# Kernel tuning notes

Measured on AMD Instinct MI355X. Metric: run time of the kernel, lower is better.

Reference implementation:

```python
import jax, jax.numpy as jnp
import numpy as np

N_NODES = 50000
N_EDGES = 800000
IN_C = 256
HID_C = 256
OUT_C = 128
N_GRAPHS = 256


def setup_inputs() -> dict:
    key = jax.random.key(0)
    ks = jax.random.split(key, 12)
    x = jax.random.normal(ks[0], (N_NODES, IN_C), dtype=jnp.float32)
    src = jax.random.randint(ks[1], (N_EDGES,), 0, N_NODES, dtype=jnp.int32)
    dst = jnp.sort(jax.random.randint(ks[2], (N_EDGES,), 0, N_NODES, dtype=jnp.int32))
    p = jax.random.uniform(ks[3], (N_NODES,), dtype=jnp.float32)
    batch = jnp.sort(jax.random.randint(ks[4], (N_NODES,), 0, N_GRAPHS, dtype=jnp.int32))
    root_ptr = jax.random.randint(ks[5], (N_GRAPHS,), 0, N_NODES, dtype=jnp.int32)
    s1 = 1.0 / np.sqrt(IN_C)
    s2 = 1.0 / np.sqrt(HID_C)
    s3 = 1.0 / np.sqrt(2 * HID_C)
    Wl1 = jax.random.uniform(ks[6], (IN_C, HID_C), jnp.float32, -s1, s1)
    Wr1 = jax.random.uniform(ks[7], (IN_C, HID_C), jnp.float32, -s1, s1)
    b1 = jnp.zeros((HID_C,), jnp.float32)
    Wl2 = jax.random.uniform(ks[8], (HID_C, HID_C), jnp.float32, -s2, s2)
    Wr2 = jax.random.uniform(ks[9], (HID_C, HID_C), jnp.float32, -s2, s2)
    b2 = jnp.zeros((HID_C,), jnp.float32)
    Wlin = jax.random.uniform(ks[10], (2 * HID_C, OUT_C), jnp.float32, -s3, s3)
    blin = jax.random.uniform(ks[11], (OUT_C,), jnp.float32, -s3, s3)
    return {"x": x, "src": src, "dst": dst, "p": p, "batch": batch,
            "root_ptr": root_ptr, "num_graphs": N_GRAPHS,
            "Wl1": Wl1, "Wr1": Wr1, "b1": b1,
            "Wl2": Wl2, "Wr2": Wr2, "b2": b2,
            "Wlin": Wlin, "blin": blin}


def _sage_conv(x, src, dst, inv_deg, Wl, Wr, b):
    # mean aggregation of neighbor features: scatter-add then divide by degree
    agg = jax.ops.segment_sum(x[src], dst, num_segments=N_NODES)  # [N, d]
    agg = agg * inv_deg[:, None]
    return agg @ Wl + x @ Wr + b


def reference(x, src, dst, p, batch, root_ptr, num_graphs,
              Wl1, Wr1, b1, Wl2, Wr2, b2, Wlin, blin):
    # in-degree for mean aggregation (shared by both convs)
    deg = jax.ops.segment_sum(jnp.ones_like(dst, dtype=x.dtype), dst,
                              num_segments=N_NODES)
    inv_deg = jnp.where(deg > 0, 1.0 / jnp.maximum(deg, 1.0), 0.0)

    h = _sage_conv(x, src, dst, inv_deg, Wl1, Wr1, b1)
    h = jax.nn.relu(h)  # dropout is identity in eval mode
    h = _sage_conv(h, src, dst, inv_deg, Wl2, Wr2, b2)

    # masked mean pool of p-weighted features per graph
    pw = h * p[:, None]
    gsum = jax.ops.segment_sum(pw, batch, num_segments=num_graphs)
    gcnt = jax.ops.segment_sum(jnp.ones_like(p), batch, num_segments=num_graphs)
    gmean = gsum / jnp.maximum(gcnt, 1.0)[:, None]

    feat = jnp.concatenate([h[root_ptr], gmean], axis=-1)  # [G, 2*hid]
    return feat @ Wlin + blin
```

## Files before the change

### kernel.cpp

```cpp
#include <hip/hip_runtime.h>
#include <hip/hip_bf16.h>

#define N_NODES 50000
#define N_EDGES 800000
#define C_DIM   256
#define OUT_C   128
#define N_GRAPHS 256

typedef unsigned short ushort8 __attribute__((ext_vector_type(8)));
typedef __bf16         bf16x8  __attribute__((ext_vector_type(8)));
typedef float          f32x4   __attribute__((ext_vector_type(4)));

typedef __attribute__((address_space(1))) const unsigned int gu32;
typedef __attribute__((address_space(3))) unsigned int lu32;

#if __has_builtin(__builtin_amdgcn_sched_barrier)
#define SCHED_FENCE() __builtin_amdgcn_sched_barrier(0)
#else
#define SCHED_FENCE() ((void)0)
#endif

__device__ __forceinline__ float us2f(unsigned short u) {
    unsigned int x = ((unsigned int)u) << 16;
    return __builtin_bit_cast(float, x);
}
__device__ __forceinline__ unsigned short f2bf(float f) {
    unsigned int u = __builtin_bit_cast(unsigned int, f);
    u += 0x7fffu + ((u >> 16) & 1u);
    return (unsigned short)(u >> 16);
}

__device__ __forceinline__ int lower_bound_i(const int* __restrict__ a, int n, int v) {
    int lo = 0, hi = n;
    while (lo < hi) {
        int mid = (lo + hi) >> 1;
        if (a[mid] < v) lo = mid + 1; else hi = mid;
    }
    return lo;
}

__global__ void build_ptrs(const int* __restrict__ dst, const int* __restrict__ batch,
                           int* __restrict__ row_ptr, int* __restrict__ graph_ptr,
                           float* __restrict__ inv_deg) {
    int i = blockIdx.x * blockDim.x + threadIdx.x;
    if (i <= N_NODES) {
        int lb = lower_bound_i(dst, N_EDGES, i);
        row_ptr[i] = lb;
        if (i < N_NODES) {
            int ub = lower_bound_i(dst, N_EDGES, i + 1);
            int cnt = ub - lb;
            inv_deg[i] = (cnt > 0) ? (1.0f / (float)cnt) : 0.0f;
        }
    }
    if (i <= N_GRAPHS) graph_ptr[i] = lower_bound_i(batch, N_NODES, i);
}

__global__ void convert_bf16(const float* __restrict__ S, unsigned short* __restrict__ D) {
    int i = blockIdx.x * blockDim.x + threadIdx.x;
    float4 v = *(const float4*)(S + ((size_t)i << 2));
    ushort4 o;
    o.x = f2bf(v.x); o.y = f2bf(v.y); o.z = f2bf(v.z); o.w = f2bf(v.w);
    *(ushort4*)(D + ((size_t)i << 2)) = o;
}

__global__ void transpose256x4(const float* __restrict__ S0, const float* __restrict__ S1,
                               const float* __restrict__ S2, const float* __restrict__ S3,
                               unsigned short* __restrict__ D0, unsigned short* __restrict__ D1,
                               unsigned short* __restrict__ D2, unsigned short* __restrict__ D3) {
    const float* S; unsigned short* D;
    switch (blockIdx.y) {
        case 0: S = S0; D = D0; break;
        case 1: S = S1; D = D1; break;
        case 2: S = S2; D = D2; break;
        default: S = S3; D = D3; break;
    }
    int i = blockIdx.x * 256 + threadIdx.x;
    int k = i >> 8, n = i & 255;
    D[n * 256 + k] = f2bf(S[i]);
}

__global__ void aggregate(const unsigned short* __restrict__ X,
                          const int* __restrict__ src,
                          const int* __restrict__ row_ptr,
                          const float* __restrict__ inv_deg,
                          unsigned short* __restrict__ out) {
    int gw   = (blockIdx.x * blockDim.x + threadIdx.x) >> 6;
    int lane = threadIdx.x & 63;
    if (gw >= N_NODES) return;
    int e0 = row_ptr[gw], e1 = row_ptr[gw + 1];
    const int lo = lane << 2;
    float a0 = 0.f, a1 = 0.f, a2 = 0.f, a3 = 0.f;
    int e = e0;

    for (; e + 16 <= e1; e += 16) {
        int sidx[16];
#pragma unroll
        for (int j = 0; j < 16; ++j) sidx[j] = src[e + j];
        ushort4 v[16];
#pragma unroll
        for (int j = 0; j < 16; ++j)
            v[j] = *(const ushort4*)(X + ((size_t)sidx[j] << 8) + lo);
        SCHED_FENCE();
#pragma unroll
        for (int j = 0; j < 16; ++j) {
            a0 += us2f(v[j].x); a1 += us2f(v[j].y);
            a2 += us2f(v[j].z); a3 += us2f(v[j].w);
        }
    }
    int rem = e1 - e;
    if (rem > 0) {
        int cl = e1 - 1;
        int sidx[16]; float w[16];
#pragma unroll
        for (int j = 0; j < 16; ++j) {
            int ej = e + j;
            int ec = ej < cl ? ej : cl;
            w[j] = (ej < e1) ? 1.0f : 0.0f;
            sidx[j] = src[ec];
        }
        ushort4 v[16];
#pragma unroll
        for (int j = 0; j < 16; ++j)
            v[j] = *(const ushort4*)(X + ((size_t)sidx[j] << 8) + lo);
        SCHED_FENCE();
#pragma unroll
        for (int j = 0; j < 16; ++j) {
            a0 = fmaf(us2f(v[j].x), w[j], a0);
            a1 = fmaf(us2f(v[j].y), w[j], a1);
            a2 = fmaf(us2f(v[j].z), w[j], a2);
            a3 = fmaf(us2f(v[j].w), w[j], a3);
        }
    }

    float sc = inv_deg[gw];
    ushort4 o;
    o.x = f2bf(a0 * sc); o.y = f2bf(a1 * sc); o.z = f2bf(a2 * sc); o.w = f2bf(a3 * sc);
    *(ushort4*)(out + ((size_t)gw << 8) + lo) = o;
}

__global__ __launch_bounds__(256, 2)
void gemm_fused(const unsigned short* __restrict__ A1,
                const unsigned short* __restrict__ A2,
                const unsigned short* __restrict__ B1t,
                const unsigned short* __restrict__ B2t,
                const float* __restrict__ bias,
                unsigned short* __restrict__ C,
                int M, int do_relu) {
    __shared__ __align__(16) unsigned short As[8192];
    __shared__ __align__(16) unsigned short Bs[8192];

    const int t    = threadIdx.x;
    const int m0   = blockIdx.x * 128;
    const int n0   = blockIdx.y * 128;
    const int lane = t & 63, wid = t >> 6;
    const int wm   = (wid >> 1) * 64;
    const int wn   = (wid & 1) * 64;
    const int lrow = lane & 15;
    const int kq   = lane >> 4;

    const f32x4 zero4 = {0.f, 0.f, 0.f, 0.f};
    f32x4 acc[4][4];
#pragma unroll
    for (int i = 0; i < 4; ++i)
#pragma unroll
        for (int j = 0; j < 4; ++j) acc[i][j] = zero4;

    for (int it = 0; it < 8; ++it) {
        const unsigned short* __restrict__ Ab = (it < 4) ? A1 : A2;
        const unsigned short* __restrict__ Bb = (it < 4) ? B1t : B2t;
        int ko = (it * 64) & 255;

#pragma unroll
        for (int i = 0; i < 4; ++i) {
            int q   = t + i * 256;
            int row = q >> 3;
            int kb  = (q & 7) ^ (row & 7);
            const unsigned short* ga = Ab + (size_t)(m0 + row) * 256 + ko + kb * 8;
            __builtin_amdgcn_global_load_lds((gu32*)ga, (lu32*)(As + q * 8), 16, 0, 0);
            const unsigned short* gb = Bb + (size_t)(n0 + row) * 256 + ko + kb * 8;
            __builtin_amdgcn_global_load_lds((gu32*)gb, (lu32*)(Bs + q * 8), 16, 0, 0);
        }
        __syncthreads();

#pragma unroll
        for (int s = 0; s < 2; ++s) {
            int kqp = s * 4 + kq;
            bf16x8 af[4], bfr[4];
#pragma unroll
            for (int mi = 0; mi < 4; ++mi) {
                int r = wm + mi * 16 + lrow;
                int slot = r * 8 + (kqp ^ (lrow & 7));
                uint4 u = *(const uint4*)(As + slot * 8);
                af[mi] = __builtin_bit_cast(bf16x8, u);
            }
#pragma unroll
            for (int ni = 0; ni < 4; ++ni) {
                int r = wn + ni * 16 + lrow;
                int slot = r * 8 + (kqp ^ (lrow & 7));
                uint4 u = *(const uint4*)(Bs + slot * 8);
                bfr[ni] = __builtin_bit_cast(bf16x8, u);
            }
#pragma unroll
            for (int mi = 0; mi < 4; ++mi)
#pragma unroll
                for (int ni = 0; ni < 4; ++ni)
                    acc[mi][ni] = __builtin_amdgcn_mfma_f32_16x16x32_bf16(
                        af[mi], bfr[ni], acc[mi][ni], 0, 0, 0);
        }
        __syncthreads();
    }

    const int rbase = (lane >> 4) * 4;
#pragma unroll
    for (int ni = 0; ni < 4; ++ni) {
        int n  = n0 + wn + ni * 16 + lrow;
        float bv = bias[n];
#pragma unroll
        for (int mi = 0; mi < 4; ++mi) {
            int mb = m0 + wm + mi * 16 + rbase;
#pragma unroll
            for (int r = 0; r < 4; ++r) {
                int m = mb + r;
                if (m < M) {
                    float v = acc[mi][ni][r] + bv;
                    if (do_relu) v = fmaxf(v, 0.f);
                    C[(size_t)m * 256 + n] = f2bf(v);
                }
            }
        }
    }
}

__global__ void pool_feat(const unsigned short* __restrict__ h2,
                          const float* __restrict__ p,
                          const int* __restrict__ graph_ptr,
                          const int* __restrict__ root_ptr,
                          float* __restrict__ feat) {
    int g = blockIdx.x;
    int c = threadIdx.x;
    int s = graph_ptr[g], e = graph_ptr[g + 1];
    float acc = 0.f;
    for (int n = s; n < e; n += 8) {
        int cl = e - 1;
        float w[8]; int nc[8];
#pragma unroll
        for (int j = 0; j < 8; ++j) {
            int nj = n + j;
            nc[j] = nj < cl ? nj : cl;
            w[j] = (nj < e) ? p[nc[j]] : 0.0f;
        }
        unsigned short v[8];
#pragma unroll
        for (int j = 0; j < 8; ++j)
            v[j] = h2[(size_t)nc[j] * 256 + c];
        SCHED_FENCE();
#pragma unroll
        for (int j = 0; j < 8; ++j)
            acc = fmaf(us2f(v[j]), w[j], acc);
    }
    float cnt = (float)(e - s);
    float gmean = acc / fmaxf(cnt, 1.0f);
    int root = root_ptr[g];
    feat[(size_t)g * 512 + c]       = us2f(h2[(size_t)root * 256 + c]);
    feat[(size_t)g * 512 + 256 + c] = gmean;
}

__global__ void final_gemm(const float* __restrict__ feat,
                           const float* __restrict__ Wlin,
                           const float* __restrict__ blin,
                           float* __restrict__ out) {
    int g = blockIdx.x;
    int o = threadIdx.x;
    __shared__ float fl[512];
    for (int k = o; k < 512; k += 128) fl[k] = feat[(size_t)g * 512 + k];
    __syncthreads();
    float s0 = 0.f, s1 = 0.f, s2 = 0.f, s3 = 0.f;
    for (int k = 0; k < 512; k += 4) {
        s0 = fmaf(fl[k + 0], Wlin[(k + 0) * 128 + o], s0);
        s1 = fmaf(fl[k + 1], Wlin[(k + 1) * 128 + o], s1);
        s2 = fmaf(fl[k + 2], Wlin[(k + 2) * 128 + o], s2);
        s3 = fmaf(fl[k + 3], Wlin[(k + 3) * 128 + o], s3);
    }
    out[(size_t)g * 128 + o] = blin[o] + ((s0 + s1) + (s2 + s3));
}

extern "C" void kernel_launch(void* const* d_in, const int* in_sizes, int n_in,
                              void* d_out, int out_size, void* d_ws, size_t ws_size,
                              hipStream_t stream) {
    const float* x        = (const float*)d_in[0];
    const int*   src      = (const int*)d_in[1];
    const int*   dst      = (const int*)d_in[2];
    const float* p        = (const float*)d_in[3];
    const int*   batch    = (const int*)d_in[4];
    const int*   root_ptr = (const int*)d_in[5];
    const float* Wl1  = (const float*)d_in[7];
    const float* Wr1  = (const float*)d_in[8];
    const float* b1   = (const float*)d_in[9];
    const float* Wl2  = (const float*)d_in[10];
    const float* Wr2  = (const float*)d_in[11];
    const float* b2   = (const float*)d_in[12];
    const float* Wlin = (const float*)d_in[13];
    const float* blin = (const float*)d_in[14];
    float* out = (float*)d_out;

    size_t off = 0;
    char* base = (char*)d_ws;
    auto alloc = [&](size_t bytes) -> void* {
        void* q = base + off;
        off += (bytes + 255) & ~(size_t)255;
        return q;
    };
    int*            row_ptr   = (int*)  alloc((N_NODES + 1) * sizeof(int));
    int*            graph_ptr = (int*)  alloc((N_GRAPHS + 1) * sizeof(int));
    float*          inv_deg   = (float*)alloc(N_NODES * sizeof(float));
    unsigned short* Wl1t = (unsigned short*)alloc(256 * 256 * 2);
    unsigned short* Wr1t = (unsigned short*)alloc(256 * 256 * 2);
    unsigned short* Wl2t = (unsigned short*)alloc(256 * 256 * 2);
    unsigned short* Wr2t = (unsigned short*)alloc(256 * 256 * 2);
    unsigned short* xb   = (unsigned short*)alloc((size_t)N_NODES * 256 * 2);
    unsigned short* aggb = (unsigned short*)alloc((size_t)N_NODES * 256 * 2);
    unsigned short* h1   = (unsigned short*)alloc((size_t)N_NODES * 256 * 2);
    unsigned short* h2   = (unsigned short*)alloc((size_t)N_NODES * 256 * 2);
    float*          feat = (float*)alloc((size_t)N_GRAPHS * 512 * sizeof(float));
    (void)ws_size; (void)n_in; (void)in_sizes; (void)out_size;

    build_ptrs<<<196, 256, 0, stream>>>(dst, batch, row_ptr, graph_ptr, inv_deg);
    convert_bf16<<<N_NODES * 256 / 4 / 256, 256, 0, stream>>>(x, xb);
    transpose256x4<<<dim3(256, 4), 256, 0, stream>>>(Wl1, Wr1, Wl2, Wr2,
                                                     Wl1t, Wr1t, Wl2t, Wr2t);

    dim3 ggrid((N_NODES + 127) / 128, 2);

    aggregate<<<N_NODES / 4, 256, 0, stream>>>(xb, src, row_ptr, inv_deg, aggb);
    gemm_fused<<<ggrid, 256, 0, stream>>>(aggb, xb, Wl1t, Wr1t, b1, h1, N_NODES, 1);

    aggregate<<<N_NODES / 4, 256, 0, stream>>>(h1, src, row_ptr, inv_deg, aggb);
    gemm_fused<<<ggrid, 256, 0, stream>>>(aggb, h1, Wl2t, Wr2t, b2, h2, N_NODES, 0);

    pool_feat<<<N_GRAPHS, 256, 0, stream>>>(h2, p, graph_ptr, root_ptr, feat);
    final_gemm<<<N_GRAPHS, 128, 0, stream>>>(feat, Wlin, blin, out);
}
```

Baseline: 345.7 us.

## Merge preprocessing kernels, use scalar edge indices, widen GEMM tile to full N

Combines the bf16 conversion, weight transpose and CSR pointer build into one preprocess launch, which removes two kernel launches. In aggregate and pool_feat, edge and node indices are made wave-uniform with readfirstlane so they can sit in scalar registers, and the index loads are interleaved with the gathers. The fused GEMM now uses 512-thread blocks that cover all 256 output columns, so the A tile is loaded once instead of once per column half. The cost is a larger LDS footprint (48KB per block) and more registers per block, which may lower occupancy.

```diff
diff --git a/kernel.cpp b/kernel.cpp
--- a/kernel.cpp
+++ b/kernel.cpp
@@ -39,44 +39,47 @@
     return lo;
 }
 
-__global__ void build_ptrs(const int* __restrict__ dst, const int* __restrict__ batch,
+__global__ void preprocess(const float* __restrict__ x, unsigned short* __restrict__ xb,
+                           const float* __restrict__ W0, const float* __restrict__ W1,
+                           const float* __restrict__ W2, const float* __restrict__ W3,
+                           unsigned short* __restrict__ D0, unsigned short* __restrict__ D1,
+                           unsigned short* __restrict__ D2, unsigned short* __restrict__ D3,
+                           const int* __restrict__ dst, const int* __restrict__ batch,
                            int* __restrict__ row_ptr, int* __restrict__ graph_ptr,
                            float* __restrict__ inv_deg) {
-    int i = blockIdx.x * blockDim.x + threadIdx.x;
-    if (i <= N_NODES) {
-        int lb = lower_bound_i(dst, N_EDGES, i);
-        row_ptr[i] = lb;
-        if (i < N_NODES) {
-            int ub = lower_bound_i(dst, N_EDGES, i + 1);
-            int cnt = ub - lb;
-            inv_deg[i] = (cnt > 0) ? (1.0f / (float)cnt) : 0.0f;
-        }
-    }
-    if (i <= N_GRAPHS) graph_ptr[i] = lower_bound_i(batch, N_NODES, i);
-}
-
-__global__ void convert_bf16(const float* __restrict__ S, unsigned short* __restrict__ D) {
-    int i = blockIdx.x * blockDim.x + threadIdx.x;
-    float4 v = *(const float4*)(S + ((size_t)i << 2));
-    ushort4 o;
-    o.x = f2bf(v.x); o.y = f2bf(v.y); o.z = f2bf(v.z); o.w = f2bf(v.w);
-    *(ushort4*)(D + ((size_t)i << 2)) = o;
-}
-
-__global__ void transpose256x4(const float* __restrict__ S0, const float* __restrict__ S1,
-                               const float* __restrict__ S2, const float* __restrict__ S3,
-                               unsigned short* __restrict__ D0, unsigned short* __restrict__ D1,
-                               unsigned short* __restrict__ D2, unsigned short* __restrict__ D3) {
-    const float* S; unsigned short* D;
-    switch (blockIdx.y) {
-        case 0: S = S0; D = D0; break;
-        case 1: S = S1; D = D1; break;
-        case 2: S = S2; D = D2; break;
-        default: S = S3; D = D3; break;
-    }
-    int i = blockIdx.x * 256 + threadIdx.x;
-    int k = i >> 8, n = i & 255;
-    D[n * 256 + k] = f2bf(S[i]);
+    int b = blockIdx.x;
+    int t = threadIdx.x;
+    if (b < 12500) {
+        int i = b * 256 + t;
+        float4 v = *(const float4*)(x + ((size_t)i << 2));
+        ushort4 o;
+        o.x = f2bf(v.x); o.y = f2bf(v.y); o.z = f2bf(v.z); o.w = f2bf(v.w);
+        *(ushort4*)(xb + ((size_t)i << 2)) = o;
+    } else if (b < 13524) {
+        int sub = b - 12500;
+        const float* S; unsigned short* D;
+        switch (sub >> 8) {
+            case 0: S = W0; D = D0; break;
+            case 1: S = W1; D = D1; break;
+            case 2: S = W2; D = D2; break;
+            default: S = W3; D = D3; break;
+        }
+        int i = (sub & 255) * 256 + t;
+        int k = i >> 8, n = i & 255;
+        D[n * 256 + k] = f2bf(S[i]);
+    } else {
+        int i = (b - 13524) * 256 + t;
+        if (i <= N_NODES) {
+            int lb = lower_bound_i(dst, N_EDGES, i);
+            row_ptr[i] = lb;
+            if (i < N_NODES) {
+                int ub = lower_bound_i(dst, N_EDGES, i + 1);
+                int cnt = ub - lb;
+                inv_deg[i] = (cnt > 0) ? (1.0f / (float)cnt) : 0.0f;
+            }
+        }
+        if (i <= N_GRAPHS) graph_ptr[i] = lower_bound_i(batch, N_NODES, i);
+    }
 }
 
 __global__ void aggregate(const unsigned short* __restrict__ X,
@@ -93,13 +96,12 @@
     int e = e0;
 
     for (; e + 16 <= e1; e += 16) {
-        int sidx[16];
-#pragma unroll
-        for (int j = 0; j < 16; ++j) sidx[j] = src[e + j];
         ushort4 v[16];
 #pragma unroll
-        for (int j = 0; j < 16; ++j)
-            v[j] = *(const ushort4*)(X + ((size_t)sidx[j] << 8) + lo);
+        for (int j = 0; j < 16; ++j) {
+            int s = __builtin_amdgcn_readfirstlane(src[e + j]);
+            v[j] = *(const ushort4*)(X + ((size_t)s << 8) + lo);
+        }
         SCHED_FENCE();
 #pragma unroll
         for (int j = 0; j < 16; ++j) {
@@ -110,18 +112,15 @@
     int rem = e1 - e;
     if (rem > 0) {
         int cl = e1 - 1;
-        int sidx[16]; float w[16];
+        ushort4 v[16]; float w[16];
 #pragma unroll
         for (int j = 0; j < 16; ++j) {
             int ej = e + j;
             int ec = ej < cl ? ej : cl;
             w[j] = (ej < e1) ? 1.0f : 0.0f;
-            sidx[j] = src[ec];
-        }
-        ushort4 v[16];
-#pragma unroll
-        for (int j = 0; j < 16; ++j)
-            v[j] = *(const ushort4*)(X + ((size_t)sidx[j] << 8) + lo);
+            int s = __builtin_amdgcn_readfirstlane(src[ec]);
+            v[j] = *(const ushort4*)(X + ((size_t)s << 8) + lo);
+        }
         SCHED_FENCE();
 #pragma unroll
         for (int j = 0; j < 16; ++j) {
@@ -138,7 +137,7 @@
     *(ushort4*)(out + ((size_t)gw << 8) + lo) = o;
 }
 
-__global__ __launch_bounds__(256, 2)
+__global__ __launch_bounds__(512, 2)
 void gemm_fused(const unsigned short* __restrict__ A1,
                 const unsigned short* __restrict__ A2,
                 const unsigned short* __restrict__ B1t,
@@ -147,14 +146,13 @@
                 unsigned short* __restrict__ C,
                 int M, int do_relu) {
     __shared__ __align__(16) unsigned short As[8192];
-    __shared__ __align__(16) unsigned short Bs[8192];
+    __shared__ __align__(16) unsigned short Bs[16384];
 
     const int t    = threadIdx.x;
     const int m0   = blockIdx.x * 128;
-    const int n0   = blockIdx.y * 128;
     const int lane = t & 63, wid = t >> 6;
-    const int wm   = (wid >> 1) * 64;
-    const int wn   = (wid & 1) * 64;
+    const int wm   = (wid >> 2) * 64;
+    const int wn   = (wid & 3) * 64;
     const int lrow = lane & 15;
     const int kq   = lane >> 4;
 
@@ -171,13 +169,19 @@
         int ko = (it * 64) & 255;
 
 #pragma unroll
-        for (int i = 0; i < 4; ++i) {
-            int q   = t + i * 256;
+        for (int i = 0; i < 2; ++i) {
+            int q   = t + i * 512;
             int row = q >> 3;
             int kb  = (q & 7) ^ (row & 7);
             const unsigned short* ga = Ab + (size_t)(m0 + row) * 256 + ko + kb * 8;
             __builtin_amdgcn_global_load_lds((gu32*)ga, (lu32*)(As + q * 8), 16, 0, 0);
-            const unsigned short* gb = Bb + (size_t)(n0 + row) * 256 + ko + kb * 8;
+        }
+#pragma unroll
+        for (int i = 0; i < 4; ++i) {
+            int q   = t + i * 512;
+            int row = q >> 3;
+            int kb  = (q & 7) ^ (row & 7);
+            const unsigned short* gb = Bb + (size_t)row * 256 + ko + kb * 8;
             __builtin_amdgcn_global_load_lds((gu32*)gb, (lu32*)(Bs + q * 8), 16, 0, 0);
         }
         __syncthreads();
@@ -213,7 +217,7 @@
     const int rbase = (lane >> 4) * 4;
 #pragma unroll
     for (int ni = 0; ni < 4; ++ni) {
-        int n  = n0 + wn + ni * 16 + lrow;
+        int n  = wn + ni * 16 + lrow;
         float bv = bias[n];
 #pragma unroll
         for (int mi = 0; mi < 4; ++mi) {
@@ -242,17 +246,15 @@
     float acc = 0.f;
     for (int n = s; n < e; n += 8) {
         int cl = e - 1;
-        float w[8]; int nc[8];
+        float w[8]; unsigned short v[8];
 #pragma unroll
         for (int j = 0; j < 8; ++j) {
             int nj = n + j;
-            nc[j] = nj < cl ? nj : cl;
-            w[j] = (nj < e) ? p[nc[j]] : 0.0f;
-        }
-        unsigned short v[8];
-#pragma unroll
-        for (int j = 0; j < 8; ++j)
-            v[j] = h2[(size_t)nc[j] * 256 + c];
+            int ncj = nj < cl ? nj : cl;
+            int nu = __builtin_amdgcn_readfirstlane(ncj);
+            w[j] = (nj < e) ? p[nu] : 0.0f;
+            v[j] = h2[(size_t)nu * 256 + c];
+        }
         SCHED_FENCE();
 #pragma unroll
         for (int j = 0; j < 8; ++j)
@@ -324,18 +326,17 @@
     float*          feat = (float*)alloc((size_t)N_GRAPHS * 512 * sizeof(float));
     (void)ws_size; (void)n_in; (void)in_sizes; (void)out_size;
 
-    build_ptrs<<<196, 256, 0, stream>>>(dst, batch, row_ptr, graph_ptr, inv_deg);
-    convert_bf16<<<N_NODES * 256 / 4 / 256, 256, 0, stream>>>(x, xb);
-    transpose256x4<<<dim3(256, 4), 256, 0, stream>>>(Wl1, Wr1, Wl2, Wr2,
-                                                     Wl1t, Wr1t, Wl2t, Wr2t);
-
-    dim3 ggrid((N_NODES + 127) / 128, 2);
+    preprocess<<<13720, 256, 0, stream>>>(x, xb, Wl1, Wr1, Wl2, Wr2,
+                                          Wl1t, Wr1t, Wl2t, Wr2t,
+                                          dst, batch, row_ptr, graph_ptr, inv_deg);
+
+    dim3 ggrid((N_NODES + 127) / 128);
 
     aggregate<<<N_NODES / 4, 256, 0, stream>>>(xb, src, row_ptr, inv_deg, aggb);
-    gemm_fused<<<ggrid, 256, 0, stream>>>(aggb, xb, Wl1t, Wr1t, b1, h1, N_NODES, 1);
+    gemm_fused<<<ggrid, 512, 0, stream>>>(aggb, xb, Wl1t, Wr1t, b1, h1, N_NODES, 1);
 
     aggregate<<<N_NODES / 4, 256, 0, stream>>>(h1, src, row_ptr, inv_deg, aggb);
-    gemm_fused<<<ggrid, 256, 0, stream>>>(aggb, h1, Wl2t, Wr2t, b2, h2, N_NODES, 0);
+    gemm_fused<<<ggrid, 512, 0, stream>>>(aggb, h1, Wl2t, Wr2t, b2, h2, N_NODES, 0);
 
     pool_feat<<<N_GRAPHS, 256, 0, stream>>>(h2, p, graph_ptr, root_ptr, feat);
     final_gemm<<<N_GRAPHS, 128, 0, stream>>>(feat, Wlin, blin, out);
```

New measurement: 327.1 us. 5.4% less time.
